# Kernel tuning notes

Hardware: AMD Instinct MI355X
Metric: run time of the kernel (lower is better)

## Reference

```python
import jax, jax.numpy as jnp
import numpy as np

N = 100000   # num_nodes
F_IN = 128   # num_features
D = 64       # encoder_dim
E = 1600000  # num raw edges (avg degree 16)
BETA = 0.01  # perturb_value


def setup_inputs() -> dict:
    key = jax.random.key(0)
    ks = jax.random.split(key, 8)
    x = jax.random.normal(ks[0], (N, F_IN), dtype=jnp.float32)
    edge_index = jax.random.randint(ks[1], (2, E), 0, N, dtype=jnp.int64)
    W1 = jax.random.normal(ks[2], (F_IN, D), dtype=jnp.float32) * 0.05
    b1 = jnp.zeros((D,), dtype=jnp.float32)
    W2 = jax.random.normal(ks[3], (D, D), dtype=jnp.float32) * 0.05
    b2 = jnp.zeros((D,), dtype=jnp.float32)
    # torch FloatTensor(...).normal_(-beta, beta): mean=-beta, std=beta
    perturb1 = jax.random.normal(ks[4], (N, D), dtype=jnp.float32) * BETA - BETA
    perturb2 = jax.random.normal(ks[5], (N, D), dtype=jnp.float32) * BETA - BETA
    return {"x": x, "edge_index": edge_index, "W1": W1, "b1": b1,
            "W2": W2, "b2": b2, "perturb1": perturb1, "perturb2": perturb2}


def _graph_conv(h, src, dst, norm, W, b):
    # linear transform then gather -> weighted message -> scatter-add
    h = h @ W                                  # [N, D]
    msg = h[src] * norm[:, None]               # [E+N, D] irregular gather
    agg = jax.ops.segment_sum(msg, dst, num_segments=N)  # scatter-add
    return agg + b


def reference(x, edge_index, W1, b1, W2, b2, perturb1, perturb2):
    # add self-loops (GCN/PPMI-style propagation with symmetric norm;
    # PPMI edge weights approximated by degree normalization)
    loops = jnp.arange(N, dtype=edge_index.dtype)
    src = jnp.concatenate([edge_index[0], loops])
    dst = jnp.concatenate([edge_index[1], loops])
    deg = jax.ops.segment_sum(jnp.ones_like(dst, dtype=x.dtype), dst, num_segments=N)
    deg = jnp.maximum(deg, 1.0)
    norm = jax.lax.rsqrt(deg[src] * deg[dst])  # [E+N]

    h = _graph_conv(x, src, dst, norm, W1, b1) + perturb1
    h = jax.nn.relu(h)                         # dropout = identity (eval mode)
    h = _graph_conv(h, src, dst, norm, W2, b2) + perturb2
    return h
```

## Files before the change

kernel.cpp:

```cpp
#include <hip/hip_runtime.h>

#define DD 64
#define FIN 128
#define BK 256
#define MAXBUK 512
#define CAP 8192
#define ESCAP 12288
#define EPB 4096

#define XS1 132
#define XS2 68

static __device__ __forceinline__ float4 f4fma(float a, float4 b, float4 c) {
    c.x = fmaf(a, b.x, c.x);
    c.y = fmaf(a, b.y, c.y);
    c.z = fmaf(a, b.z, c.z);
    c.w = fmaf(a, b.w, c.w);
    return c;
}

static __device__ __forceinline__ unsigned bfpack(float lo, float hi) {
    unsigned ul = __float_as_uint(lo);
    unsigned uh = __float_as_uint(hi);
    ul += 0x7fffu + ((ul >> 16) & 1u);
    uh += 0x7fffu + ((uh >> 16) & 1u);
    return (ul >> 16) | (uh & 0xffff0000u);
}

static __device__ __forceinline__ void bfacc(uint4 v, float* a) {
    a[0] += __uint_as_float(v.x << 16);
    a[1] += __uint_as_float(v.x & 0xffff0000u);
    a[2] += __uint_as_float(v.y << 16);
    a[3] += __uint_as_float(v.y & 0xffff0000u);
    a[4] += __uint_as_float(v.z << 16);
    a[5] += __uint_as_float(v.z & 0xffff0000u);
    a[6] += __uint_as_float(v.w << 16);
    a[7] += __uint_as_float(v.w & 0xffff0000u);
}

__global__ __launch_bounds__(256) void k_bucket(const int* __restrict__ src,
                                                const int* __restrict__ dst,
                                                unsigned* __restrict__ buf,
                                                int* __restrict__ gcur,
                                                int E, int nbuk) {
    __shared__ int hist[MAXBUK];
    __shared__ int base[MAXBUK];
    int e0 = blockIdx.x * EPB;
    int e1 = min(e0 + EPB, E);
    int dreg[16];
#pragma unroll
    for (int i = 0; i < 16; ++i) {
        int e = e0 + threadIdx.x + i * 256;
        dreg[i] = (e < e1) ? dst[e] : -1;
    }
    for (int i = threadIdx.x; i < nbuk; i += 256) hist[i] = 0;
    __syncthreads();
#pragma unroll
    for (int i = 0; i < 16; ++i)
        if (dreg[i] >= 0) atomicAdd(&hist[dreg[i] >> 8], 1);
    __syncthreads();
    for (int i = threadIdx.x; i < nbuk; i += 256) {
        int c = hist[i];
        base[i] = c ? atomicAdd(&gcur[i], c) : 0;
        hist[i] = 0;
    }
    __syncthreads();
#pragma unroll
    for (int i = 0; i < 16; ++i) {
        int d = dreg[i];
        if (d >= 0) {
            int e = e0 + threadIdx.x + i * 256;
            int b = d >> 8;
            int off = base[b] + atomicAdd(&hist[b], 1);
            if (off < CAP)
                buf[(size_t)b * CAP + off] = ((unsigned)src[e] << 8) | ((unsigned)d & 255u);
        }
    }
}

__global__ __launch_bounds__(256) void k_csr(const unsigned* __restrict__ buf,
                                             const int* __restrict__ gcur,
                                             int* __restrict__ rowptr,
                                             int* __restrict__ lenp,
                                             float* __restrict__ rs,
                                             int* __restrict__ es, int n, int dummy) {
    __shared__ int cnt[BK];
    __shared__ int excl[BK];
    __shared__ int cur[BK];
    __shared__ int wsum[4];
    int b = blockIdx.x;
    int tid = threadIdx.x;
    int lane = tid & 63, wid = tid >> 6;
    cnt[tid] = 0;
    cur[tid] = 0;
    __syncthreads();
    int count = gcur[b];
    const unsigned* rec = buf + (size_t)b * CAP;
    for (int i = tid; i < count; i += 256)
        atomicAdd(&cnt[rec[i] & (BK - 1)], 1);
    __syncthreads();
    int v = cnt[tid];
    int pv = (v + 15) & ~15;
    int s = pv;
    for (int off = 1; off < 64; off <<= 1) {
        int t = __shfl_up(s, off, 64);
        if (lane >= off) s += t;
    }
    if (lane == 63) wsum[wid] = s;
    __syncthreads();
    int wo = 0;
    for (int w = 0; w < wid; ++w) wo += wsum[w];
    excl[tid] = s - pv + wo;
    __syncthreads();
    int node = b * BK + tid;
    int base = b * ESCAP;
    if (node < n) {
        rowptr[node] = base + excl[tid];
        lenp[node] = pv;
        rs[node] = rsqrtf((float)(v + 1));
    }
    for (int i = tid; i < count; i += 256) {
        unsigned r = rec[i];
        int local = r & (BK - 1);
        int pos = base + excl[local] + atomicAdd(&cur[local], 1);
        es[pos] = (int)(r >> 8);
    }
    int st = base + excl[tid];
    for (int i = v; i < pv; ++i) es[st + i] = dummy;
}

__global__ __launch_bounds__(256) void k_gemm1(const float* __restrict__ x,
                                               const float* __restrict__ W,
                                               const float* __restrict__ rs,
                                               unsigned* __restrict__ hpb, int n) {
    __shared__ float sx[64 * XS1];
    __shared__ float sW[FIN * DD];
    int row0 = blockIdx.x * 64;
    for (int i = threadIdx.x; i < FIN * DD / 4; i += 256)
        ((float4*)sW)[i] = ((const float4*)W)[i];
    for (int i = threadIdx.x; i < 64 * FIN / 4; i += 256) {
        int r = i >> 5;
        int c = i & 31;
        int row = row0 + r;
        float4 v = make_float4(0.f, 0.f, 0.f, 0.f);
        if (row < n) v = *(const float4*)(x + (size_t)row * FIN + c * 4);
        *(float4*)(sx + r * XS1 + c * 4) = v;
    }
    __syncthreads();
    int col4 = (threadIdx.x & 15) * 4;
    int rowg = threadIdx.x >> 4;
    float4 acc[4] = {make_float4(0,0,0,0), make_float4(0,0,0,0),
                     make_float4(0,0,0,0), make_float4(0,0,0,0)};
#pragma unroll 8
    for (int k = 0; k < FIN; k += 4) {
        float4 w0 = *(const float4*)(sW + k * DD + col4);
        float4 w1 = *(const float4*)(sW + (k + 1) * DD + col4);
        float4 w2 = *(const float4*)(sW + (k + 2) * DD + col4);
        float4 w3 = *(const float4*)(sW + (k + 3) * DD + col4);
#pragma unroll
        for (int r = 0; r < 4; ++r) {
            float4 xv = *(const float4*)(sx + (rowg * 4 + r) * XS1 + k);
            acc[r] = f4fma(xv.x, w0, acc[r]);
            acc[r] = f4fma(xv.y, w1, acc[r]);
            acc[r] = f4fma(xv.z, w2, acc[r]);
            acc[r] = f4fma(xv.w, w3, acc[r]);
        }
    }
#pragma unroll
    for (int r = 0; r < 4; ++r) {
        int row = row0 + rowg * 4 + r;
        uint2 pk = make_uint2(0u, 0u);
        if (row < n) {
            float sc = rs[row];
            pk.x = bfpack(acc[r].x * sc, acc[r].y * sc);
            pk.y = bfpack(acc[r].z * sc, acc[r].w * sc);
        }
        *(uint2*)(hpb + (size_t)row * 32 + (col4 >> 1)) = pk;
    }
}

__global__ __launch_bounds__(256) void k_gemm2(const float* __restrict__ a,
                                               const float* __restrict__ W,
                                               const float* __restrict__ rs,
                                               unsigned* __restrict__ hpb, int n) {
    __shared__ float sx[64 * XS2];
    __shared__ float sW[DD * DD];
    int row0 = blockIdx.x * 64;
    for (int i = threadIdx.x; i < DD * DD / 4; i += 256)
        ((float4*)sW)[i] = ((const float4*)W)[i];
    for (int i = threadIdx.x; i < 64 * DD / 4; i += 256) {
        int r = i >> 4;
        int c = i & 15;
        int row = row0 + r;
        float4 v = make_float4(0.f, 0.f, 0.f, 0.f);
        if (row < n) {
            v = *(const float4*)(a + (size_t)row * DD + c * 4);
            v.x = fmaxf(v.x, 0.f); v.y = fmaxf(v.y, 0.f);
            v.z = fmaxf(v.z, 0.f); v.w = fmaxf(v.w, 0.f);
        }
        *(float4*)(sx + r * XS2 + c * 4) = v;
    }
    __syncthreads();
    int col4 = (threadIdx.x & 15) * 4;
    int rowg = threadIdx.x >> 4;
    float4 acc[4] = {make_float4(0,0,0,0), make_float4(0,0,0,0),
                     make_float4(0,0,0,0), make_float4(0,0,0,0)};
#pragma unroll 8
    for (int k = 0; k < DD; k += 4) {
        float4 w0 = *(const float4*)(sW + k * DD + col4);
        float4 w1 = *(const float4*)(sW + (k + 1) * DD + col4);
        float4 w2 = *(const float4*)(sW + (k + 2) * DD + col4);
        float4 w3 = *(const float4*)(sW + (k + 3) * DD + col4);
#pragma unroll
        for (int r = 0; r < 4; ++r) {
            float4 xv = *(const float4*)(sx + (rowg * 4 + r) * XS2 + k);
            acc[r] = f4fma(xv.x, w0, acc[r]);
            acc[r] = f4fma(xv.y, w1, acc[r]);
            acc[r] = f4fma(xv.z, w2, acc[r]);
            acc[r] = f4fma(xv.w, w3, acc[r]);
        }
    }
#pragma unroll
    for (int r = 0; r < 4; ++r) {
        int row = row0 + rowg * 4 + r;
        uint2 pk = make_uint2(0u, 0u);
        if (row < n) {
            float sc = rs[row];
            pk.x = bfpack(acc[r].x * sc, acc[r].y * sc);
            pk.y = bfpack(acc[r].z * sc, acc[r].w * sc);
        }
        *(uint2*)(hpb + (size_t)row * 32 + (col4 >> 1)) = pk;
    }
}

__global__ __launch_bounds__(256) void k_agg(const uint4* __restrict__ hp4,
                                             const int* __restrict__ es,
                                             const int* __restrict__ rowptr,
                                             const int* __restrict__ lenp,
                                             const float* __restrict__ rs,
                                             const float* __restrict__ b,
                                             const float* __restrict__ pert,
                                             float* __restrict__ outp, int n) {
    int lane = threadIdx.x & 63;
    int wv = threadIdx.x >> 6;
    int g = lane >> 4;
    int sub = lane & 15;
    int eslot = sub >> 3;
    int q = sub & 7;
    int node = (blockIdx.x * 4 + wv) * 4 + g;
    bool alive = node < n;
    int nc = alive ? node : 0;
    int e0 = rowptr[nc];
    int len = alive ? lenp[nc] : 0;
    float A[8] = {0,0,0,0,0,0,0,0};
    float B[8] = {0,0,0,0,0,0,0,0};
    float C[8] = {0,0,0,0,0,0,0,0};
    float D[8] = {0,0,0,0,0,0,0,0};
    if (alive && eslot == 0) bfacc(hp4[(size_t)nc * 8 + q], A);
    for (int eb = e0; eb < e0 + len; eb += 16) {
        int idx = es[eb + sub];
        int i0 = __shfl(idx, 0 + eslot, 16);
        int i1 = __shfl(idx, 2 + eslot, 16);
        int i2 = __shfl(idx, 4 + eslot, 16);
        int i3 = __shfl(idx, 6 + eslot, 16);
        int i4 = __shfl(idx, 8 + eslot, 16);
        int i5 = __shfl(idx, 10 + eslot, 16);
        int i6 = __shfl(idx, 12 + eslot, 16);
        int i7 = __shfl(idx, 14 + eslot, 16);
        uint4 v0 = hp4[(size_t)i0 * 8 + q];
        uint4 v1 = hp4[(size_t)i1 * 8 + q];
        uint4 v2 = hp4[(size_t)i2 * 8 + q];
        uint4 v3 = hp4[(size_t)i3 * 8 + q];
        uint4 v4 = hp4[(size_t)i4 * 8 + q];
        uint4 v5 = hp4[(size_t)i5 * 8 + q];
        uint4 v6 = hp4[(size_t)i6 * 8 + q];
        uint4 v7 = hp4[(size_t)i7 * 8 + q];
        bfacc(v0, A); bfacc(v1, B); bfacc(v2, C); bfacc(v3, D);
        bfacc(v4, A); bfacc(v5, B); bfacc(v6, C); bfacc(v7, D);
    }
#pragma unroll
    for (int j = 0; j < 8; ++j) {
        float v = (A[j] + B[j]) + (C[j] + D[j]);
        v += __shfl_xor(v, 8, 64);
        A[j] = v;
    }
    if (alive && eslot == 0) {
        float r = rs[nc];
        size_t o = (size_t)nc * DD + q * 8;
        float4 p0 = *(const float4*)(pert + o);
        float4 p1 = *(const float4*)(pert + o + 4);
        float4 b0 = *(const float4*)(b + q * 8);
        float4 b1 = *(const float4*)(b + q * 8 + 4);
        float4 r0, r1;
        r0.x = fmaf(r, A[0], b0.x + p0.x);
        r0.y = fmaf(r, A[1], b0.y + p0.y);
        r0.z = fmaf(r, A[2], b0.z + p0.z);
        r0.w = fmaf(r, A[3], b0.w + p0.w);
        r1.x = fmaf(r, A[4], b1.x + p1.x);
        r1.y = fmaf(r, A[5], b1.y + p1.y);
        r1.z = fmaf(r, A[6], b1.z + p1.z);
        r1.w = fmaf(r, A[7], b1.w + p1.w);
        *(float4*)(outp + o) = r0;
        *(float4*)(outp + o + 4) = r1;
    }
}

extern "C" void kernel_launch(void* const* d_in, const int* in_sizes, int n_in,
                              void* d_out, int out_size, void* d_ws, size_t ws_size,
                              hipStream_t stream) {
    const float* x  = (const float*)d_in[0];
    const int*   ei = (const int*)d_in[1];
    const float* W1 = (const float*)d_in[2];
    const float* b1 = (const float*)d_in[3];
    const float* W2 = (const float*)d_in[4];
    const float* b2 = (const float*)d_in[5];
    const float* p1 = (const float*)d_in[6];
    const float* p2 = (const float*)d_in[7];
    float* out = (float*)d_out;

    int n = in_sizes[0] / FIN;
    int E = in_sizes[1] / 2;
    const int* src = ei;
    const int* dst = ei + E;
    int nbuk = (n + BK - 1) / BK;
    int gb = (n + 63) / 64;

    char* ws = (char*)d_ws;
    size_t off = 0;
    int* gcur   = (int*)(ws + off); off += sizeof(int) * MAXBUK;
    int* rowptr = (int*)(ws + off); off += sizeof(int) * (size_t)n;
    int* lenp   = (int*)(ws + off); off += sizeof(int) * (size_t)n;
    float* rs   = (float*)(ws + off); off += sizeof(float) * (size_t)n;
    int* es     = (int*)(ws + off); off += sizeof(int) * (size_t)nbuk * ESCAP;
    off = (off + 15) & ~(size_t)15;
    unsigned* buf = (unsigned*)(ws + off);
    off += sizeof(unsigned) * (size_t)nbuk * CAP;
    off = (off + 15) & ~(size_t)15;
    unsigned* hpb = (unsigned*)(ws + off);
    off += (size_t)gb * 64 * 128;
    float* agg1 = (float*)(ws + off); off += sizeof(float) * (size_t)n * DD;

    int ab = (n + 15) / 16;
    int bb = (E + EPB - 1) / EPB;

    hipMemsetAsync(gcur, 0, sizeof(int) * MAXBUK, stream);
    k_bucket<<<bb, 256, 0, stream>>>(src, dst, buf, gcur, E, nbuk);
    k_csr<<<nbuk, 256, 0, stream>>>(buf, gcur, rowptr, lenp, rs, es, n, n);

    k_gemm1<<<gb, 256, 0, stream>>>(x, W1, rs, hpb, n);
    k_agg<<<ab, 256, 0, stream>>>((const uint4*)hpb, es, rowptr, lenp, rs, b1, p1, agg1, n);

    k_gemm2<<<gb, 256, 0, stream>>>(agg1, W2, rs, hpb, n);
    k_agg<<<ab, 256, 0, stream>>>((const uint4*)hpb, es, rowptr, lenp, rs, b2, p2, out, n);
}
```

Before: 180.3 us.

## Use fp16 MFMA for both dense transforms and store features as fp16

Replaces the scalar fp32 FMA GEMMs with 16x16x32 f16 MFMA instructions. A new prep kernel converts W1 and W2 to transposed fp16 so each lane loads its B fragments straight from global memory. Inputs are converted to fp16 in shared memory, and the scaled outputs are staged through shared memory for coalesced stores. The gathered feature table changes from bf16 to fp16, which gives more mantissa bits but less range, and it adds one single-block kernel launch.

```diff
diff --git a/kernel.cpp b/kernel.cpp
--- a/kernel.cpp
+++ b/kernel.cpp
@@ -8,34 +8,16 @@
 #define ESCAP 12288
 #define EPB 4096
 
-#define XS1 132
-#define XS2 68
-
-static __device__ __forceinline__ float4 f4fma(float a, float4 b, float4 c) {
-    c.x = fmaf(a, b.x, c.x);
-    c.y = fmaf(a, b.y, c.y);
-    c.z = fmaf(a, b.z, c.z);
-    c.w = fmaf(a, b.w, c.w);
-    return c;
-}
-
-static __device__ __forceinline__ unsigned bfpack(float lo, float hi) {
-    unsigned ul = __float_as_uint(lo);
-    unsigned uh = __float_as_uint(hi);
-    ul += 0x7fffu + ((ul >> 16) & 1u);
-    uh += 0x7fffu + ((uh >> 16) & 1u);
-    return (ul >> 16) | (uh & 0xffff0000u);
-}
-
-static __device__ __forceinline__ void bfacc(uint4 v, float* a) {
-    a[0] += __uint_as_float(v.x << 16);
-    a[1] += __uint_as_float(v.x & 0xffff0000u);
-    a[2] += __uint_as_float(v.y << 16);
-    a[3] += __uint_as_float(v.y & 0xffff0000u);
-    a[4] += __uint_as_float(v.z << 16);
-    a[5] += __uint_as_float(v.z & 0xffff0000u);
-    a[6] += __uint_as_float(v.w << 16);
-    a[7] += __uint_as_float(v.w & 0xffff0000u);
+typedef _Float16 half8 __attribute__((ext_vector_type(8)));
+typedef float f32x4 __attribute__((ext_vector_type(4)));
+
+static __device__ __forceinline__ void f16acc(uint4 v, float* a) {
+    union { unsigned u; _Float16 h[2]; } t0, t1, t2, t3;
+    t0.u = v.x; t1.u = v.y; t2.u = v.z; t3.u = v.w;
+    a[0] += (float)t0.h[0]; a[1] += (float)t0.h[1];
+    a[2] += (float)t1.h[0]; a[3] += (float)t1.h[1];
+    a[4] += (float)t2.h[0]; a[5] += (float)t2.h[1];
+    a[6] += (float)t3.h[0]; a[7] += (float)t3.h[1];
 }
 
 __global__ __launch_bounds__(256) void k_bucket(const int* __restrict__ src,
@@ -129,107 +111,132 @@
     for (int i = v; i < pv; ++i) es[st + i] = dummy;
 }
 
+__global__ __launch_bounds__(256) void k_prep(const float* __restrict__ W1,
+                                              const float* __restrict__ W2,
+                                              _Float16* __restrict__ Wt1,
+                                              _Float16* __restrict__ Wt2) {
+    int tid = threadIdx.x;
+    for (int i = tid; i < FIN * DD; i += 256) {
+        int k = i >> 6, c = i & 63;
+        Wt1[c * FIN + k] = (_Float16)W1[i];
+    }
+    for (int i = tid; i < DD * DD; i += 256) {
+        int k = i >> 6, c = i & 63;
+        Wt2[c * DD + k] = (_Float16)W2[i];
+    }
+}
+
 __global__ __launch_bounds__(256) void k_gemm1(const float* __restrict__ x,
-                                               const float* __restrict__ W,
+                                               const _Float16* __restrict__ Wt,
                                                const float* __restrict__ rs,
-                                               unsigned* __restrict__ hpb, int n) {
-    __shared__ float sx[64 * XS1];
-    __shared__ float sW[FIN * DD];
+                                               _Float16* __restrict__ hpf, int n) {
+    __shared__ _Float16 sx[64 * 136];
     int row0 = blockIdx.x * 64;
-    for (int i = threadIdx.x; i < FIN * DD / 4; i += 256)
-        ((float4*)sW)[i] = ((const float4*)W)[i];
-    for (int i = threadIdx.x; i < 64 * FIN / 4; i += 256) {
-        int r = i >> 5;
-        int c = i & 31;
+    int tid = threadIdx.x;
+    for (int i = tid; i < 2048; i += 256) {
+        int r = i >> 5, c = i & 31;
         int row = row0 + r;
         float4 v = make_float4(0.f, 0.f, 0.f, 0.f);
         if (row < n) v = *(const float4*)(x + (size_t)row * FIN + c * 4);
-        *(float4*)(sx + r * XS1 + c * 4) = v;
-    }
-    __syncthreads();
-    int col4 = (threadIdx.x & 15) * 4;
-    int rowg = threadIdx.x >> 4;
-    float4 acc[4] = {make_float4(0,0,0,0), make_float4(0,0,0,0),
-                     make_float4(0,0,0,0), make_float4(0,0,0,0)};
-#pragma unroll 8
-    for (int k = 0; k < FIN; k += 4) {
-        float4 w0 = *(const float4*)(sW + k * DD + col4);
-        float4 w1 = *(const float4*)(sW + (k + 1) * DD + col4);
-        float4 w2 = *(const float4*)(sW + (k + 2) * DD + col4);
-        float4 w3 = *(const float4*)(sW + (k + 3) * DD + col4);
-#pragma unroll
-        for (int r = 0; r < 4; ++r) {
-            float4 xv = *(const float4*)(sx + (rowg * 4 + r) * XS1 + k);
-            acc[r] = f4fma(xv.x, w0, acc[r]);
-            acc[r] = f4fma(xv.y, w1, acc[r]);
-            acc[r] = f4fma(xv.z, w2, acc[r]);
-            acc[r] = f4fma(xv.w, w3, acc[r]);
-        }
-    }
-#pragma unroll
-    for (int r = 0; r < 4; ++r) {
-        int row = row0 + rowg * 4 + r;
-        uint2 pk = make_uint2(0u, 0u);
-        if (row < n) {
-            float sc = rs[row];
-            pk.x = bfpack(acc[r].x * sc, acc[r].y * sc);
-            pk.y = bfpack(acc[r].z * sc, acc[r].w * sc);
-        }
-        *(uint2*)(hpb + (size_t)row * 32 + (col4 >> 1)) = pk;
-    }
-}
-
-__global__ __launch_bounds__(256) void k_gemm2(const float* __restrict__ a,
-                                               const float* __restrict__ W,
+        union { _Float16 h[4]; uint2 u; } t;
+        t.h[0] = (_Float16)v.x; t.h[1] = (_Float16)v.y;
+        t.h[2] = (_Float16)v.z; t.h[3] = (_Float16)v.w;
+        *(uint2*)(sx + r * 136 + c * 4) = t.u;
+    }
+    __syncthreads();
+    int lane = tid & 63, wave = tid >> 6;
+    int r15 = lane & 15, g = lane >> 4;
+    half8 a[4];
+    const _Float16* ap = sx + (wave * 16 + r15) * 136 + g * 8;
+#pragma unroll
+    for (int kc = 0; kc < 4; ++kc) a[kc] = *(const half8*)(ap + kc * 32);
+    half8 bfr[4][4];
+    const _Float16* bp = Wt + (size_t)r15 * FIN + g * 8;
+#pragma unroll
+    for (int ct = 0; ct < 4; ++ct)
+#pragma unroll
+        for (int kc = 0; kc < 4; ++kc)
+            bfr[ct][kc] = *(const half8*)(bp + ct * 16 * FIN + kc * 32);
+    f32x4 acc[4] = {{0.f,0.f,0.f,0.f},{0.f,0.f,0.f,0.f},{0.f,0.f,0.f,0.f},{0.f,0.f,0.f,0.f}};
+#pragma unroll
+    for (int ct = 0; ct < 4; ++ct)
+#pragma unroll
+        for (int kc = 0; kc < 4; ++kc)
+            acc[ct] = __builtin_amdgcn_mfma_f32_16x16x32_f16(a[kc], bfr[ct][kc], acc[ct], 0, 0, 0);
+    __syncthreads();
+#pragma unroll
+    for (int reg = 0; reg < 4; ++reg) {
+        int rowl = wave * 16 + g * 4 + reg;
+        int row = row0 + rowl;
+        float sc = (row < n) ? rs[row] : 0.f;
+#pragma unroll
+        for (int ct = 0; ct < 4; ++ct)
+            sx[rowl * 72 + ct * 16 + r15] = (_Float16)(acc[ct][reg] * sc);
+    }
+    __syncthreads();
+    for (int i = tid; i < 1024; i += 256) {
+        int r = i >> 4, q = i & 15;
+        uint2 v = *(const uint2*)(sx + r * 72 + q * 4);
+        *(uint2*)(hpf + (size_t)(row0 + r) * DD + q * 4) = v;
+    }
+}
+
+__global__ __launch_bounds__(256) void k_gemm2(const float* __restrict__ ain,
+                                               const _Float16* __restrict__ Wt,
                                                const float* __restrict__ rs,
-                                               unsigned* __restrict__ hpb, int n) {
-    __shared__ float sx[64 * XS2];
-    __shared__ float sW[DD * DD];
+                                               _Float16* __restrict__ hpf, int n) {
+    __shared__ _Float16 sx[64 * 72];
     int row0 = blockIdx.x * 64;
-    for (int i = threadIdx.x; i < DD * DD / 4; i += 256)
-        ((float4*)sW)[i] = ((const float4*)W)[i];
-    for (int i = threadIdx.x; i < 64 * DD / 4; i += 256) {
-        int r = i >> 4;
-        int c = i & 15;
+    int tid = threadIdx.x;
+    for (int i = tid; i < 1024; i += 256) {
+        int r = i >> 4, c = i & 15;
         int row = row0 + r;
         float4 v = make_float4(0.f, 0.f, 0.f, 0.f);
         if (row < n) {
-            v = *(const float4*)(a + (size_t)row * DD + c * 4);
+            v = *(const float4*)(ain + (size_t)row * DD + c * 4);
             v.x = fmaxf(v.x, 0.f); v.y = fmaxf(v.y, 0.f);
             v.z = fmaxf(v.z, 0.f); v.w = fmaxf(v.w, 0.f);
         }
-        *(float4*)(sx + r * XS2 + c * 4) = v;
-    }
-    __syncthreads();
-    int col4 = (threadIdx.x & 15) * 4;
-    int rowg = threadIdx.x >> 4;
-    float4 acc[4] = {make_float4(0,0,0,0), make_float4(0,0,0,0),
-                     make_float4(0,0,0,0), make_float4(0,0,0,0)};
-#pragma unroll 8
-    for (int k = 0; k < DD; k += 4) {
-        float4 w0 = *(const float4*)(sW + k * DD + col4);
-        float4 w1 = *(const float4*)(sW + (k + 1) * DD + col4);
-        float4 w2 = *(const float4*)(sW + (k + 2) * DD + col4);
-        float4 w3 = *(const float4*)(sW + (k + 3) * DD + col4);
-#pragma unroll
-        for (int r = 0; r < 4; ++r) {
-            float4 xv = *(const float4*)(sx + (rowg * 4 + r) * XS2 + k);
-            acc[r] = f4fma(xv.x, w0, acc[r]);
-            acc[r] = f4fma(xv.y, w1, acc[r]);
-            acc[r] = f4fma(xv.z, w2, acc[r]);
-            acc[r] = f4fma(xv.w, w3, acc[r]);
-        }
-    }
-#pragma unroll
-    for (int r = 0; r < 4; ++r) {
-        int row = row0 + rowg * 4 + r;
-        uint2 pk = make_uint2(0u, 0u);
-        if (row < n) {
-            float sc = rs[row];
-            pk.x = bfpack(acc[r].x * sc, acc[r].y * sc);
-            pk.y = bfpack(acc[r].z * sc, acc[r].w * sc);
-        }
-        *(uint2*)(hpb + (size_t)row * 32 + (col4 >> 1)) = pk;
+        union { _Float16 h[4]; uint2 u; } t;
+        t.h[0] = (_Float16)v.x; t.h[1] = (_Float16)v.y;
+        t.h[2] = (_Float16)v.z; t.h[3] = (_Float16)v.w;
+        *(uint2*)(sx + r * 72 + c * 4) = t.u;
+    }
+    __syncthreads();
+    int lane = tid & 63, wave = tid >> 6;
+    int r15 = lane & 15, g = lane >> 4;
+    half8 a[2];
+    const _Float16* ap = sx + (wave * 16 + r15) * 72 + g * 8;
+#pragma unroll
+    for (int kc = 0; kc < 2; ++kc) a[kc] = *(const half8*)(ap + kc * 32);
+    half8 bfr[4][2];
+    const _Float16* bp = Wt + (size_t)r15 * DD + g * 8;
+#pragma unroll
+    for (int ct = 0; ct < 4; ++ct)
+#pragma unroll
+        for (int kc = 0; kc < 2; ++kc)
+            bfr[ct][kc] = *(const half8*)(bp + ct * 16 * DD + kc * 32);
+    f32x4 acc[4] = {{0.f,0.f,0.f,0.f},{0.f,0.f,0.f,0.f},{0.f,0.f,0.f,0.f},{0.f,0.f,0.f,0.f}};
+#pragma unroll
+    for (int ct = 0; ct < 4; ++ct)
+#pragma unroll
+        for (int kc = 0; kc < 2; ++kc)
+            acc[ct] = __builtin_amdgcn_mfma_f32_16x16x32_f16(a[kc], bfr[ct][kc], acc[ct], 0, 0, 0);
+    __syncthreads();
+#pragma unroll
+    for (int reg = 0; reg < 4; ++reg) {
+        int rowl = wave * 16 + g * 4 + reg;
+        int row = row0 + rowl;
+        float sc = (row < n) ? rs[row] : 0.f;
+#pragma unroll
+        for (int ct = 0; ct < 4; ++ct)
+            sx[rowl * 72 + ct * 16 + r15] = (_Float16)(acc[ct][reg] * sc);
+    }
+    __syncthreads();
+    for (int i = tid; i < 1024; i += 256) {
+        int r = i >> 4, q = i & 15;
+        uint2 v = *(const uint2*)(sx + r * 72 + q * 4);
+        *(uint2*)(hpf + (size_t)(row0 + r) * DD + q * 4) = v;
     }
 }
 
@@ -256,7 +263,7 @@
     float B[8] = {0,0,0,0,0,0,0,0};
     float C[8] = {0,0,0,0,0,0,0,0};
     float D[8] = {0,0,0,0,0,0,0,0};
-    if (alive && eslot == 0) bfacc(hp4[(size_t)nc * 8 + q], A);
+    if (alive && eslot == 0) f16acc(hp4[(size_t)nc * 8 + q], A);
     for (int eb = e0; eb < e0 + len; eb += 16) {
         int idx = es[eb + sub];
         int i0 = __shfl(idx, 0 + eslot, 16);
@@ -275,8 +282,8 @@
         uint4 v5 = hp4[(size_t)i5 * 8 + q];
         uint4 v6 = hp4[(size_t)i6 * 8 + q];
         uint4 v7 = hp4[(size_t)i7 * 8 + q];
-        bfacc(v0, A); bfacc(v1, B); bfacc(v2, C); bfacc(v3, D);
-        bfacc(v4, A); bfacc(v5, B); bfacc(v6, C); bfacc(v7, D);
+        f16acc(v0, A); f16acc(v1, B); f16acc(v2, C); f16acc(v3, D);
+        f16acc(v4, A); f16acc(v5, B); f16acc(v6, C); f16acc(v7, D);
     }
 #pragma unroll
     for (int j = 0; j < 8; ++j) {
@@ -336,20 +343,25 @@
     unsigned* buf = (unsigned*)(ws + off);
     off += sizeof(unsigned) * (size_t)nbuk * CAP;
     off = (off + 15) & ~(size_t)15;
-    unsigned* hpb = (unsigned*)(ws + off);
-    off += (size_t)gb * 64 * 128;
+    _Float16* hpf = (_Float16*)(ws + off);
+    off += (size_t)gb * 64 * DD * 2;
+    off = (off + 15) & ~(size_t)15;
+    _Float16* Wt1 = (_Float16*)(ws + off); off += FIN * DD * 2;
+    _Float16* Wt2 = (_Float16*)(ws + off); off += DD * DD * 2;
+    off = (off + 15) & ~(size_t)15;
     float* agg1 = (float*)(ws + off); off += sizeof(float) * (size_t)n * DD;
 
     int ab = (n + 15) / 16;
     int bb = (E + EPB - 1) / EPB;
 
     hipMemsetAsync(gcur, 0, sizeof(int) * MAXBUK, stream);
+    k_prep<<<1, 256, 0, stream>>>(W1, W2, Wt1, Wt2);
     k_bucket<<<bb, 256, 0, stream>>>(src, dst, buf, gcur, E, nbuk);
     k_csr<<<nbuk, 256, 0, stream>>>(buf, gcur, rowptr, lenp, rs, es, n, n);
 
-    k_gemm1<<<gb, 256, 0, stream>>>(x, W1, rs, hpb, n);
-    k_agg<<<ab, 256, 0, stream>>>((const uint4*)hpb, es, rowptr, lenp, rs, b1, p1, agg1, n);
-
-    k_gemm2<<<gb, 256, 0, stream>>>(agg1, W2, rs, hpb, n);
-    k_agg<<<ab, 256, 0, stream>>>((const uint4*)hpb, es, rowptr, lenp, rs, b2, p2, out, n);
-}
+    k_gemm1<<<gb, 256, 0, stream>>>(x, Wt1, rs, hpf, n);
+    k_agg<<<ab, 256, 0, stream>>>((const uint4*)hpf, es, rowptr, lenp, rs, b1, p1, agg1, n);
+
+    k_gemm2<<<gb, 256, 0, stream>>>(agg1, Wt2, rs, hpf, n);
+    k_agg<<<ab, 256, 0, stream>>>((const uint4*)hpf, es, rowptr, lenp, rs, b2, p2, out, n);
+}
```

Result: faster. 168.6 us (-6.5%).
